# Optimization experiments

Hardware: AMD Instinct MI355X
Metric: run time of the kernel (lower is better)

The kernel has to match this reference:

```python
import jax, jax.numpy as jnp
import numpy as np

INPUT_DIM1 = 512
INPUT_DIM2 = 512
OUTPUT_DIM = 8192


def _make_sketch(seed_h, seed_s, input_dim, output_dim):
    # Faithful to torch module: dense [input_dim, output_dim] matrix with one
    # nonzero (+-1) per row at column rand_h[i].
    np.random.seed(seed_h)
    rand_h = np.random.randint(output_dim, size=input_dim)
    np.random.seed(seed_s)
    rand_s = (2 * np.random.randint(2, size=input_dim) - 1).astype(np.float32)
    M = np.zeros((input_dim, output_dim), dtype=np.float32)
    M[np.arange(input_dim), rand_h] = rand_s
    return jnp.asarray(M)


def setup_inputs() -> dict:
    key = jax.random.key(0)
    k1, k2 = jax.random.split(key)
    bottom1 = jax.random.normal(k1, (32, INPUT_DIM1, 14, 14), dtype=jnp.float32)
    bottom2 = jax.random.normal(k2, (32, INPUT_DIM2, 14, 14), dtype=jnp.float32)
    S1 = _make_sketch(1, 3, INPUT_DIM1, OUTPUT_DIM)
    S2 = _make_sketch(5, 7, INPUT_DIM2, OUTPUT_DIM)
    return {"bottom1": bottom1, "bottom2": bottom2, "S1": S1, "S2": S2}


def reference(bottom1, bottom2, S1, S2):
    B, _, H, W = bottom1.shape
    d = S1.shape[1]
    # [B, C, H, W] -> [B*H*W, C]
    b1 = jnp.transpose(bottom1, (0, 2, 3, 1)).reshape(-1, bottom1.shape[1])
    b2 = jnp.transpose(bottom2, (0, 2, 3, 1)).reshape(-1, bottom2.shape[1])
    sketch1 = b1 @ S1  # [N, d]
    sketch2 = b2 @ S2
    fft1 = jnp.fft.fft(sketch1, axis=-1)
    fft2 = jnp.fft.fft(sketch2, axis=-1)
    cbp_flat = jnp.real(jnp.fft.ifft(fft1 * fft2, axis=-1))
    cbp = cbp_flat.reshape(B, H, W, d)
    return cbp.sum(axis=(1, 2))  # sum_pool=True -> [B, d]
```

## Files before the change

kernel.cpp:

```cpp
#include <hip/hip_runtime.h>


#define D     8192
#define DMASK 8191
#define C     512
#define HW    196
#define NB    32
#define LDK   40
#define NCH   7
#define NSL   32

typedef __attribute__((ext_vector_type(8))) short bf16x8;
typedef __attribute__((ext_vector_type(4))) float f32x4;

__device__ __forceinline__ unsigned short f2bf(float f, unsigned xm) {
    unsigned u = __float_as_uint(f) ^ xm;
    return (unsigned short)((u + 0x7fffu + ((u >> 16) & 1u)) >> 16);
}

__global__ __launch_bounds__(256) void extract2(
    const float* __restrict__ S1, const float* __restrict__ S2,
    int* __restrict__ h1, float* __restrict__ s1,
    int* __restrict__ h2, float* __restrict__ s2)
{
    const int  row   = blockIdx.x & 511;
    const bool first = blockIdx.x < 512;
    const float* S = first ? S1 : S2;
    const float4* rp = (const float4*)(S + (size_t)row * D);
    const int tid = threadIdx.x;

    float4 v[8];
    #pragma unroll
    for (int ii = 0; ii < 8; ++ii) v[ii] = rp[tid + 256 * ii];

    float ssum = 0.f, wsum = 0.f;
    #pragma unroll
    for (int ii = 0; ii < 8; ++ii) {
        const float base = (float)(4 * (tid + 256 * ii));
        ssum += (v[ii].x + v[ii].y) + (v[ii].z + v[ii].w);
        wsum += v[ii].x * base + v[ii].y * (base + 1.f)
              + v[ii].z * (base + 2.f) + v[ii].w * (base + 3.f);
    }
    #pragma unroll
    for (int off = 32; off; off >>= 1) {
        ssum += __shfl_down(ssum, off, 64);
        wsum += __shfl_down(wsum, off, 64);
    }
    __shared__ float rs[4], rw[4];
    if ((tid & 63) == 0) { rs[tid >> 6] = ssum; rw[tid >> 6] = wsum; }
    __syncthreads();
    if (tid == 0) {
        const float st = (rs[0] + rs[1]) + (rs[2] + rs[3]);
        const float wt = (rw[0] + rw[1]) + (rw[2] + rw[3]);
        if (first) { h1[row] = (int)(wt * st); s1[row] = st; }
        else       { h2[row] = (int)(wt * st); s2[row] = st; }
    }
}

__global__ __launch_bounds__(256, 3) void cbp_mfma(
    const float* __restrict__ b1, const float* __restrict__ b2,
    const int* __restrict__ h1, const float* __restrict__ s1,
    const int* __restrict__ h2, const float* __restrict__ s2,
    float* __restrict__ P)
{
    const int id = blockIdx.x;
    const int b  = id & 31;
    const int m  = id >> 5;
    const int t1 = m >> 2;
    const int t2 = m & 3;

    __shared__ float hist[D];
    __shared__ __align__(16) unsigned short As[64 * LDK];
    __shared__ __align__(16) unsigned short Bs[128 * LDK];
    __shared__ int h1t[64], h2t[128];

    const int tid = threadIdx.x;

    #pragma unroll
    for (int i = 0; i < 8; ++i) {
        float4 z = {0.f, 0.f, 0.f, 0.f};
        ((float4*)hist)[tid + 256 * i] = z;
    }
    if (tid < 64)  h1t[tid] = h1[t1 * 64 + tid];
    if (tid < 128) h2t[tid] = h2[t2 * 128 + tid];

    const int ra = tid >> 2;
    const int ka = (tid & 3) * 8;
    const int rb = tid >> 1;
    const int kb = (tid & 1) * 16;

    const float* Abase = b1 + ((size_t)b * C + t1 * 64 + ra) * HW;
    const float* Bbase = b2 + ((size_t)b * C + t2 * 128 + rb) * HW;

    const unsigned am = (s1[t1 * 64  + ra] < 0.f) ? 0x80000000u : 0u;
    const unsigned bm = (s2[t2 * 128 + rb] < 0.f) ? 0x80000000u : 0u;

    float4 pva[2], pvb[4];
    pva[0] = *(const float4*)(Abase + ka);
    pva[1] = *(const float4*)(Abase + ka + 4);
    #pragma unroll
    for (int t = 0; t < 4; ++t)
        pvb[t] = *(const float4*)(Bbase + kb + 4 * t);

    const int lane  = tid & 63;
    const int w     = tid >> 6;
    const int ln15  = lane & 15;
    const int qd    = lane >> 4;
    const int koff  = qd * 8;
    const int mbase = (w >> 1) * 32;
    const int nbase = (w & 1) * 64;

    f32x4 acc[2][4] = {};

    for (int ch = 0; ch < NCH; ++ch) {
        {
            uint2 u0, u1;
            u0.x = (unsigned)f2bf(pva[0].x, am) | ((unsigned)f2bf(pva[0].y, am) << 16);
            u0.y = (unsigned)f2bf(pva[0].z, am) | ((unsigned)f2bf(pva[0].w, am) << 16);
            u1.x = (unsigned)f2bf(pva[1].x, am) | ((unsigned)f2bf(pva[1].y, am) << 16);
            u1.y = (unsigned)f2bf(pva[1].z, am) | ((unsigned)f2bf(pva[1].w, am) << 16);
            *(uint2*)&As[ra * LDK + ka]     = u0;
            *(uint2*)&As[ra * LDK + ka + 4] = u1;
            #pragma unroll
            for (int t = 0; t < 2; ++t) {
                uint2 ub;
                ub.x = (unsigned)f2bf(pvb[2*t].x, bm) | ((unsigned)f2bf(pvb[2*t].y, bm) << 16);
                ub.y = (unsigned)f2bf(pvb[2*t].z, bm) | ((unsigned)f2bf(pvb[2*t].w, bm) << 16);
                *(uint2*)&Bs[rb * LDK + kb + 8 * t] = ub;
                uint2 uc;
                uc.x = (unsigned)f2bf(pvb[2*t+1].x, bm) | ((unsigned)f2bf(pvb[2*t+1].y, bm) << 16);
                uc.y = (unsigned)f2bf(pvb[2*t+1].z, bm) | ((unsigned)f2bf(pvb[2*t+1].w, bm) << 16);
                *(uint2*)&Bs[rb * LDK + kb + 8 * t + 4] = uc;
            }
        }
        __syncthreads();

        if (ch + 1 < NCH) {
            const int gk = (ch + 1) * 32;
            const float4 z = {0.f, 0.f, 0.f, 0.f};
            const int gka = gk + ka;
            pva[0] = (gka + 4 <= HW) ? *(const float4*)(Abase + gka)     : z;
            pva[1] = (gka + 8 <= HW) ? *(const float4*)(Abase + gka + 4) : z;
            #pragma unroll
            for (int t = 0; t < 4; ++t) {
                const int gkb = gk + kb + 4 * t;
                pvb[t] = (gkb + 4 <= HW) ? *(const float4*)(Bbase + gkb) : z;
            }
        }

        bf16x8 av[2], bv[4];
        #pragma unroll
        for (int i = 0; i < 2; ++i)
            av[i] = *(const bf16x8*)&As[(mbase + i * 16 + ln15) * LDK + koff];
        #pragma unroll
        for (int j = 0; j < 4; ++j)
            bv[j] = *(const bf16x8*)&Bs[(nbase + j * 16 + ln15) * LDK + koff];
        #pragma unroll
        for (int i = 0; i < 2; ++i)
            #pragma unroll
            for (int j = 0; j < 4; ++j)
                acc[i][j] = __builtin_amdgcn_mfma_f32_16x16x32_bf16(
                    av[i], bv[j], acc[i][j], 0, 0, 0);
        __syncthreads();
    }

    int p2v[4];
    #pragma unroll
    for (int j = 0; j < 4; ++j)
        p2v[j] = h2t[nbase + j * 16 + ln15];

    #pragma unroll
    for (int i = 0; i < 2; ++i)
        #pragma unroll
        for (int qq = 0; qq < 4; ++qq) {
            const int p1 = h1t[mbase + i * 16 + qd * 4 + qq];
            #pragma unroll
            for (int j = 0; j < 4; ++j)
                unsafeAtomicAdd(&hist[(p1 + p2v[j]) & DMASK], acc[i][j][qq]);
        }

    __syncthreads();

    float* Pslice = P + (size_t)(b * NSL + m) * D;
    #pragma unroll
    for (int i = 0; i < 8; ++i)
        ((float4*)Pslice)[tid + 256 * i] = ((const float4*)hist)[tid + 256 * i];
}

__global__ __launch_bounds__(256) void reduce32(
    const float* __restrict__ P, float* __restrict__ out)
{
    const int idx4 = blockIdx.x * 256 + threadIdx.x;
    const int b    = idx4 >> 11;
    const int d4   = idx4 & 2047;

    const float4* base = (const float4*)(P + (size_t)b * NSL * D) + d4;
    float4 acc = base[0];
    #pragma unroll
    for (int s = 1; s < NSL; ++s) {
        float4 v = base[s * (D / 4)];
        acc.x += v.x; acc.y += v.y; acc.z += v.z; acc.w += v.w;
    }
    ((float4*)out)[idx4] = acc;
}

extern "C" void kernel_launch(void* const* d_in, const int* in_sizes, int n_in,
                              void* d_out, int out_size, void* d_ws, size_t ws_size,
                              hipStream_t stream)
{
    const float* bottom1 = (const float*)d_in[0];
    const float* bottom2 = (const float*)d_in[1];
    const float* S1      = (const float*)d_in[2];
    const float* S2      = (const float*)d_in[3];
    float* out = (float*)d_out;

    float* P  = (float*)d_ws;
    int*   h1 = (int*)(P + (size_t)NB * NSL * D);
    int*   h2 = h1 + C;
    float* s1 = (float*)(h2 + C);
    float* s2 = s1 + C;

    extract2<<<1024, 256, 0, stream>>>(S1, S2, h1, s1, h2, s2);
    cbp_mfma<<<1024, 256, 0, stream>>>(bottom1, bottom2,
                                       h1, s1, h2, s2, P);
    reduce32<<<256, 256, 0, stream>>>(P, out);
}
```

Before: 160.9 us.

## Loop over all A tiles per block to cut partial-histogram slices from 32 to 8

Each block now owns one 64-row B tile and loops over all eight 64-row A tiles, accumulating into one shared histogram. The partial-sum buffer shrinks from 32 to 8 slices per batch, which reduces global writes and the work in the final reduction. In exchange the grid drops from 1024 to 256 blocks, which lowers occupancy and parallelism on a many-CU GPU, and B rows are reloaded once per A tile.

```diff
diff --git a/kernel.cpp b/kernel.cpp
--- a/kernel.cpp
+++ b/kernel.cpp
@@ -8,7 +8,8 @@
 #define NB    32
 #define LDK   40
 #define NCH   7
-#define NSL   32
+#define NT1   8
+#define NSL   8
 
 typedef __attribute__((ext_vector_type(8))) short bf16x8;
 typedef __attribute__((ext_vector_type(4))) float f32x4;
@@ -65,14 +66,13 @@
 {
     const int id = blockIdx.x;
     const int b  = id & 31;
-    const int m  = id >> 5;
-    const int t1 = m >> 2;
-    const int t2 = m & 3;
+    const int t2 = id >> 5;
 
     __shared__ float hist[D];
     __shared__ __align__(16) unsigned short As[64 * LDK];
-    __shared__ __align__(16) unsigned short Bs[128 * LDK];
-    __shared__ int h1t[64], h2t[128];
+    __shared__ __align__(16) unsigned short Bs[64 * LDK];
+    __shared__ int h1a[C];
+    __shared__ int h2t[64];
 
     const int tid = threadIdx.x;
 
@@ -81,26 +81,15 @@
         float4 z = {0.f, 0.f, 0.f, 0.f};
         ((float4*)hist)[tid + 256 * i] = z;
     }
-    if (tid < 64)  h1t[tid] = h1[t1 * 64 + tid];
-    if (tid < 128) h2t[tid] = h2[t2 * 128 + tid];
-
-    const int ra = tid >> 2;
-    const int ka = (tid & 3) * 8;
-    const int rb = tid >> 1;
-    const int kb = (tid & 1) * 16;
-
-    const float* Abase = b1 + ((size_t)b * C + t1 * 64 + ra) * HW;
-    const float* Bbase = b2 + ((size_t)b * C + t2 * 128 + rb) * HW;
-
-    const unsigned am = (s1[t1 * 64  + ra] < 0.f) ? 0x80000000u : 0u;
-    const unsigned bm = (s2[t2 * 128 + rb] < 0.f) ? 0x80000000u : 0u;
-
-    float4 pva[2], pvb[4];
-    pva[0] = *(const float4*)(Abase + ka);
-    pva[1] = *(const float4*)(Abase + ka + 4);
-    #pragma unroll
-    for (int t = 0; t < 4; ++t)
-        pvb[t] = *(const float4*)(Bbase + kb + 4 * t);
+    h1a[tid]       = h1[tid];
+    h1a[tid + 256] = h1[tid + 256];
+    if (tid < 64) h2t[tid] = h2[t2 * 64 + tid];
+
+    const int r  = tid >> 2;
+    const int kc = (tid & 3) * 8;
+
+    const float* Bbase = b2 + ((size_t)b * C + t2 * 64 + r) * HW;
+    const unsigned bm  = (s2[t2 * 64 + r] < 0.f) ? 0x80000000u : 0u;
 
     const int lane  = tid & 63;
     const int w     = tid >> 6;
@@ -108,86 +97,92 @@
     const int qd    = lane >> 4;
     const int koff  = qd * 8;
     const int mbase = (w >> 1) * 32;
-    const int nbase = (w & 1) * 64;
-
-    f32x4 acc[2][4] = {};
-
-    for (int ch = 0; ch < NCH; ++ch) {
-        {
-            uint2 u0, u1;
-            u0.x = (unsigned)f2bf(pva[0].x, am) | ((unsigned)f2bf(pva[0].y, am) << 16);
-            u0.y = (unsigned)f2bf(pva[0].z, am) | ((unsigned)f2bf(pva[0].w, am) << 16);
-            u1.x = (unsigned)f2bf(pva[1].x, am) | ((unsigned)f2bf(pva[1].y, am) << 16);
-            u1.y = (unsigned)f2bf(pva[1].z, am) | ((unsigned)f2bf(pva[1].w, am) << 16);
-            *(uint2*)&As[ra * LDK + ka]     = u0;
-            *(uint2*)&As[ra * LDK + ka + 4] = u1;
-            #pragma unroll
-            for (int t = 0; t < 2; ++t) {
-                uint2 ub;
-                ub.x = (unsigned)f2bf(pvb[2*t].x, bm) | ((unsigned)f2bf(pvb[2*t].y, bm) << 16);
-                ub.y = (unsigned)f2bf(pvb[2*t].z, bm) | ((unsigned)f2bf(pvb[2*t].w, bm) << 16);
-                *(uint2*)&Bs[rb * LDK + kb + 8 * t] = ub;
-                uint2 uc;
-                uc.x = (unsigned)f2bf(pvb[2*t+1].x, bm) | ((unsigned)f2bf(pvb[2*t+1].y, bm) << 16);
-                uc.y = (unsigned)f2bf(pvb[2*t+1].z, bm) | ((unsigned)f2bf(pvb[2*t+1].w, bm) << 16);
-                *(uint2*)&Bs[rb * LDK + kb + 8 * t + 4] = uc;
+    const int nbase = (w & 1) * 32;
+
+    const float* Abase = b1 + ((size_t)b * C + r) * HW;
+    float4 pva[2], pvb[2];
+    pva[0] = *(const float4*)(Abase + kc);
+    pva[1] = *(const float4*)(Abase + kc + 4);
+    pvb[0] = *(const float4*)(Bbase + kc);
+    pvb[1] = *(const float4*)(Bbase + kc + 4);
+
+    for (int t1 = 0; t1 < NT1; ++t1) {
+        const unsigned am = (s1[t1 * 64 + r] < 0.f) ? 0x80000000u : 0u;
+
+        f32x4 acc[2][2] = {};
+
+        for (int ch = 0; ch < NCH; ++ch) {
+            {
+                uint4 ua, ub;
+                ua.x = (unsigned)f2bf(pva[0].x, am) | ((unsigned)f2bf(pva[0].y, am) << 16);
+                ua.y = (unsigned)f2bf(pva[0].z, am) | ((unsigned)f2bf(pva[0].w, am) << 16);
+                ua.z = (unsigned)f2bf(pva[1].x, am) | ((unsigned)f2bf(pva[1].y, am) << 16);
+                ua.w = (unsigned)f2bf(pva[1].z, am) | ((unsigned)f2bf(pva[1].w, am) << 16);
+                ub.x = (unsigned)f2bf(pvb[0].x, bm) | ((unsigned)f2bf(pvb[0].y, bm) << 16);
+                ub.y = (unsigned)f2bf(pvb[0].z, bm) | ((unsigned)f2bf(pvb[0].w, bm) << 16);
+                ub.z = (unsigned)f2bf(pvb[1].x, bm) | ((unsigned)f2bf(pvb[1].y, bm) << 16);
+                ub.w = (unsigned)f2bf(pvb[1].z, bm) | ((unsigned)f2bf(pvb[1].w, bm) << 16);
+                *(uint4*)&As[r * LDK + kc] = ua;
+                *(uint4*)&Bs[r * LDK + kc] = ub;
             }
+            __syncthreads();
+
+            if (ch + 1 < NCH) {
+                const int gk = (ch + 1) * 32 + kc;
+                const float4 z = {0.f, 0.f, 0.f, 0.f};
+                pva[0] = (gk + 4 <= HW) ? *(const float4*)(Abase + gk)     : z;
+                pva[1] = (gk + 8 <= HW) ? *(const float4*)(Abase + gk + 4) : z;
+                pvb[0] = (gk + 4 <= HW) ? *(const float4*)(Bbase + gk)     : z;
+                pvb[1] = (gk + 8 <= HW) ? *(const float4*)(Bbase + gk + 4) : z;
+            } else if (t1 + 1 < NT1) {
+                Abase = b1 + ((size_t)b * C + (t1 + 1) * 64 + r) * HW;
+                pva[0] = *(const float4*)(Abase + kc);
+                pva[1] = *(const float4*)(Abase + kc + 4);
+                pvb[0] = *(const float4*)(Bbase + kc);
+                pvb[1] = *(const float4*)(Bbase + kc + 4);
+            }
+
+            bf16x8 av[2], bv[2];
+            #pragma unroll
+            for (int i = 0; i < 2; ++i)
+                av[i] = *(const bf16x8*)&As[(mbase + i * 16 + ln15) * LDK + koff];
+            #pragma unroll
+            for (int j = 0; j < 2; ++j)
+                bv[j] = *(const bf16x8*)&Bs[(nbase + j * 16 + ln15) * LDK + koff];
+            #pragma unroll
+            for (int i = 0; i < 2; ++i)
+                #pragma unroll
+                for (int j = 0; j < 2; ++j)
+                    acc[i][j] = __builtin_amdgcn_mfma_f32_16x16x32_bf16(
+                        av[i], bv[j], acc[i][j], 0, 0, 0);
+            __syncthreads();
         }
-        __syncthreads();
-
-        if (ch + 1 < NCH) {
-            const int gk = (ch + 1) * 32;
-            const float4 z = {0.f, 0.f, 0.f, 0.f};
-            const int gka = gk + ka;
-            pva[0] = (gka + 4 <= HW) ? *(const float4*)(Abase + gka)     : z;
-            pva[1] = (gka + 8 <= HW) ? *(const float4*)(Abase + gka + 4) : z;
-            #pragma unroll
-            for (int t = 0; t < 4; ++t) {
-                const int gkb = gk + kb + 4 * t;
-                pvb[t] = (gkb + 4 <= HW) ? *(const float4*)(Bbase + gkb) : z;
-            }
-        }
-
-        bf16x8 av[2], bv[4];
+
+        int p2v[2];
+        #pragma unroll
+        for (int j = 0; j < 2; ++j)
+            p2v[j] = h2t[nbase + j * 16 + ln15];
+
         #pragma unroll
         for (int i = 0; i < 2; ++i)
-            av[i] = *(const bf16x8*)&As[(mbase + i * 16 + ln15) * LDK + koff];
-        #pragma unroll
-        for (int j = 0; j < 4; ++j)
-            bv[j] = *(const bf16x8*)&Bs[(nbase + j * 16 + ln15) * LDK + koff];
-        #pragma unroll
-        for (int i = 0; i < 2; ++i)
-            #pragma unroll
-            for (int j = 0; j < 4; ++j)
-                acc[i][j] = __builtin_amdgcn_mfma_f32_16x16x32_bf16(
-                    av[i], bv[j], acc[i][j], 0, 0, 0);
-        __syncthreads();
-    }
-
-    int p2v[4];
-    #pragma unroll
-    for (int j = 0; j < 4; ++j)
-        p2v[j] = h2t[nbase + j * 16 + ln15];
-
-    #pragma unroll
-    for (int i = 0; i < 2; ++i)
-        #pragma unroll
-        for (int qq = 0; qq < 4; ++qq) {
-            const int p1 = h1t[mbase + i * 16 + qd * 4 + qq];
-            #pragma unroll
-            for (int j = 0; j < 4; ++j)
-                unsafeAtomicAdd(&hist[(p1 + p2v[j]) & DMASK], acc[i][j][qq]);
-        }
+            #pragma unroll
+            for (int qq = 0; qq < 4; ++qq) {
+                const int p1 = h1a[t1 * 64 + mbase + i * 16 + qd * 4 + qq];
+                #pragma unroll
+                for (int j = 0; j < 2; ++j)
+                    unsafeAtomicAdd(&hist[(p1 + p2v[j]) & DMASK], acc[i][j][qq]);
+            }
+    }
 
     __syncthreads();
 
-    float* Pslice = P + (size_t)(b * NSL + m) * D;
+    float* Pslice = P + (size_t)(b * NSL + t2) * D;
     #pragma unroll
     for (int i = 0; i < 8; ++i)
         ((float4*)Pslice)[tid + 256 * i] = ((const float4*)hist)[tid + 256 * i];
 }
 
-__global__ __launch_bounds__(256) void reduce32(
+__global__ __launch_bounds__(256) void reduce8(
     const float* __restrict__ P, float* __restrict__ out)
 {
     const int idx4 = blockIdx.x * 256 + threadIdx.x;
@@ -221,7 +216,7 @@
     float* s2 = s1 + C;
 
     extract2<<<1024, 256, 0, stream>>>(S1, S2, h1, s1, h2, s2);
-    cbp_mfma<<<1024, 256, 0, stream>>>(bottom1, bottom2,
-                                       h1, s1, h2, s2, P);
-    reduce32<<<256, 256, 0, stream>>>(P, out);
-}
+    cbp_mfma<<<256, 256, 0, stream>>>(bottom1, bottom2,
+                                      h1, s1, h2, s2, P);
+    reduce8<<<256, 256, 0, stream>>>(P, out);
+}
```

After: 170.1 us. 5.7% more time.
